# Optimization experiments

Measured on AMD Instinct MI355X. Metric: run time of the kernel, lower is better.

## Reference

```python
import jax, jax.numpy as jnp
import numpy as np

DIM = 768
B, N = 8, 2048
TEMPERATURE = 3.0


def setup_inputs() -> dict:
    key = jax.random.key(0)
    ks = jax.random.split(key, 5)
    lim = 1.0 / np.sqrt(DIM)
    x = jax.random.normal(ks[0], (B, N, DIM), dtype=jnp.float32)
    # torch Linear params: weight [out, in], bias [out]
    w_qkv = jax.random.uniform(ks[1], (3 * DIM, DIM), minval=-lim, maxval=lim, dtype=jnp.float32)
    b_qkv = jax.random.uniform(ks[2], (3 * DIM,), minval=-lim, maxval=lim, dtype=jnp.float32)
    w_proj = jax.random.uniform(ks[3], (DIM, DIM), minval=-lim, maxval=lim, dtype=jnp.float32)
    b_proj = jax.random.uniform(ks[4], (DIM,), minval=-lim, maxval=lim, dtype=jnp.float32)
    return {"x": x, "w_qkv": w_qkv, "b_qkv": b_qkv, "w_proj": w_proj, "b_proj": b_proj}


def reference(x, w_qkv, b_qkv, w_proj, b_proj):
    scale = DIM ** (-0.5)
    qkv = jnp.einsum('bnd,ed->bne', x, w_qkv) + b_qkv  # [b, n, 3*dim]
    q, k, v = jnp.split(qkv, 3, axis=-1)
    scores = jnp.einsum('bnd,bmd->bnm', q, k) * scale  # [b, n, n]
    attn = jax.nn.softmax(scores / TEMPERATURE, axis=-1)
    # dropout p=0.0 -> identity
    out = jnp.einsum('bnm,bmd->bnd', attn, v)
    return jnp.einsum('bnd,ed->bne', out, w_proj) + b_proj
```

## Files before the change

kernel.cpp:

```cpp
#include <hip/hip_runtime.h>
#include <hip/hip_bf16.h>
#include <math.h>

#define B_BATCH 8
#define SEQ 2048
#define DIM 768
#define E3 2304

typedef __bf16 bf16x8 __attribute__((ext_vector_type(8)));
typedef float floatx4 __attribute__((ext_vector_type(4)));

__device__ __forceinline__ void load_lds_16B(const __hip_bfloat16* g, __hip_bfloat16* l) {
    __builtin_amdgcn_global_load_lds((const __attribute__((address_space(1))) void*)g,
                                     (__attribute__((address_space(3))) void*)l, 16, 0, 0);
}

template<typename T> __device__ __forceinline__ T to_out(float v);
template<> __device__ __forceinline__ float to_out<float>(float v) { return v; }
template<> __device__ __forceinline__ __hip_bfloat16 to_out<__hip_bfloat16>(float v) { return __float2bfloat16(v); }

__global__ __launch_bounds__(256, 4)
void cvt_f32_bf16(const float* __restrict__ in, __hip_bfloat16* __restrict__ out, long n8)
{
    const long i = (long)blockIdx.x * blockDim.x + threadIdx.x;
    if (i >= n8) return;
    const float4* p = (const float4*)in + i * 2;
    const float4 a = p[0], b = p[1];
    union { uint4 u; __hip_bfloat16 h[8]; } t;
    t.h[0] = __float2bfloat16(a.x); t.h[1] = __float2bfloat16(a.y);
    t.h[2] = __float2bfloat16(a.z); t.h[3] = __float2bfloat16(a.w);
    t.h[4] = __float2bfloat16(b.x); t.h[5] = __float2bfloat16(b.y);
    t.h[6] = __float2bfloat16(b.z); t.h[7] = __float2bfloat16(b.w);
    ((uint4*)out)[i] = t.u;
}

__global__ __launch_bounds__(256, 4)
void transpose64(const __hip_bfloat16* __restrict__ in, long ldi, long si,
                 __hip_bfloat16* __restrict__ out, long ldo, long so)
{
    __shared__ __hip_bfloat16 t[64][65];
    in  += (long)blockIdx.z * si;
    out += (long)blockIdx.z * so;
    const int r0 = blockIdx.x * 64;
    const int c0 = blockIdx.y * 64;
    const int tid = threadIdx.x;
    const int r  = tid >> 3;
    const int c8 = (tid & 7) * 8;
#pragma unroll
    for (int h = 0; h < 2; ++h) {
        const int row = r + h * 32;
        union { uint4 u; __hip_bfloat16 v[8]; } tmp;
        tmp.u = *(const uint4*)(in + (long)(r0 + row) * ldi + c0 + c8);
#pragma unroll
        for (int j = 0; j < 8; ++j) t[row][c8 + j] = tmp.v[j];
    }
    __syncthreads();
#pragma unroll
    for (int h = 0; h < 2; ++h) {
        const int cr = r + h * 32;
        union { uint4 u; __hip_bfloat16 v[8]; } tmp;
#pragma unroll
        for (int j = 0; j < 8; ++j) tmp.v[j] = t[c8 + j][cr];
        *(uint4*)(out + (long)(c0 + cr) * ldo + r0 + c8) = tmp.u;
    }
}

template<typename OutT, int EPI>
__global__ __launch_bounds__(256, 2)
void gemm128(const __hip_bfloat16* __restrict__ A, long lda, long sA,
             const __hip_bfloat16* __restrict__ Bm, long ldb, long sB,
             OutT* __restrict__ C, long ldc, long sC,
             const float* __restrict__ bias, float scale, int K,
             int MB, int NB)
{
    __shared__ __hip_bfloat16 As[128 * 32];
    __shared__ __hip_bfloat16 Bs[128 * 32];
    __shared__ float lsum[128];

    const int id    = blockIdx.x;
    const int xcd   = id & 7;
    const int jj    = id >> 3;
    const int pairs = gridDim.x / NB;
    const int ppx   = pairs >> 3;
    const int pair  = xcd * ppx + jj / NB;
    const int nblk  = jj % NB;
    const int zblk  = pair / MB;
    const int mblk  = pair % MB;

    A  += (long)zblk * sA;
    Bm += (long)zblk * sB;
    C  += (long)zblk * sC;

    const int n0   = nblk * 128;
    const int m0   = mblk * 128;
    const int tid  = threadIdx.x;
    const int wave = tid >> 6;
    const int lane = tid & 63;
    const int wm   = (wave & 1) * 64;
    const int wn   = (wave >> 1) * 64;

    const int sr = lane >> 2;
    const int sc = (lane & 3) * 8;

    const int fr = lane & 15;
    const int fk = (lane >> 4) * 8;

    floatx4 acc[4][4] = {};
    float rsum[4] = {0.f, 0.f, 0.f, 0.f};

    for (int k0 = 0; k0 < K; k0 += 32) {
#pragma unroll
        for (int c = 0; c < 2; ++c) {
            const int chunk = wave * 2 + c;
            const int row   = chunk * 16 + sr;
            load_lds_16B(A  + (long)(m0 + row) * lda + (k0 + sc), As + chunk * 512);
            load_lds_16B(Bm + (long)(n0 + row) * ldb + (k0 + sc), Bs + chunk * 512);
        }
        __syncthreads();

        bf16x8 af[4], bfr[4];
#pragma unroll
        for (int i = 0; i < 4; ++i) {
            af[i]  = *(const bf16x8*)(As + (wm + i * 16 + fr) * 32 + fk);
            bfr[i] = *(const bf16x8*)(Bs + (wn + i * 16 + fr) * 32 + fk);
        }
        if constexpr (EPI == 2) {
#pragma unroll
            for (int mi = 0; mi < 4; ++mi)
#pragma unroll
                for (int j = 0; j < 8; ++j)
                    rsum[mi] += (float)af[mi][j];
        }
#pragma unroll
        for (int mi = 0; mi < 4; ++mi)
#pragma unroll
            for (int ni = 0; ni < 4; ++ni)
                acc[mi][ni] = __builtin_amdgcn_mfma_f32_16x16x32_bf16(
                    af[mi], bfr[ni], acc[mi][ni], 0, 0, 0);
        __syncthreads();
    }

    if constexpr (EPI == 2) {
#pragma unroll
        for (int mi = 0; mi < 4; ++mi) {
            rsum[mi] += __shfl_xor(rsum[mi], 16, 64);
            rsum[mi] += __shfl_xor(rsum[mi], 32, 64);
        }
        if (wave < 2 && (lane >> 4) == 0) {
#pragma unroll
            for (int mi = 0; mi < 4; ++mi)
                lsum[wm + mi * 16 + (lane & 15)] = rsum[mi];
        }
        __syncthreads();
    }

    const int cr = (lane >> 4) * 4;
    const int cc = lane & 15;

    float inv[4][4];
    if constexpr (EPI == 2) {
#pragma unroll
        for (int mi = 0; mi < 4; ++mi)
#pragma unroll
            for (int r = 0; r < 4; ++r)
                inv[mi][r] = 1.0f / lsum[wm + mi * 16 + cr + r];
    }

#pragma unroll
    for (int ni = 0; ni < 4; ++ni) {
        const int col = n0 + wn + ni * 16 + cc;
        const float bv = (EPI == 0 && bias) ? bias[col] : 0.0f;
#pragma unroll
        for (int mi = 0; mi < 4; ++mi) {
#pragma unroll
            for (int r = 0; r < 4; ++r) {
                const int row = m0 + wm + mi * 16 + cr + r;
                float v = acc[mi][ni][r];
                if constexpr (EPI == 0)      v = v * scale + bv;
                else if constexpr (EPI == 1) v = __expf(v * scale);
                else                         v = v * inv[mi][r];
                C[(long)row * ldc + col] = to_out<OutT>(v);
            }
        }
    }
}

extern "C" void kernel_launch(void* const* d_in, const int* in_sizes, int n_in,
                              void* d_out, int out_size, void* d_ws, size_t ws_size,
                              hipStream_t stream)
{
    const float* x     = (const float*)d_in[0];
    const float* w_qkv = (const float*)d_in[1];
    const float* b_qkv = (const float*)d_in[2];
    const float* w_prj = (const float*)d_in[3];
    const float* b_prj = (const float*)d_in[4];
    float* out = (float*)d_out;

    const float alpha = 1.0f / (sqrtf((float)DIM) * 3.0f);

    const size_t XE   = (size_t)B_BATCH * SEQ * DIM;
    const size_t WQE  = (size_t)E3 * DIM;
    const size_t WPE  = (size_t)DIM * DIM;
    const size_t QKVE = (size_t)B_BATCH * SEQ * E3;
    const size_t SE   = (size_t)B_BATCH * SEQ * SEQ;
    const size_t OE   = XE;
    dim3 blk(256);

    const size_t full_bytes = (XE + WQE + WPE + QKVE + SE + OE) * sizeof(__hip_bfloat16);

    if (ws_size >= full_bytes) {
        __hip_bfloat16* xb  = (__hip_bfloat16*)d_ws;
        __hip_bfloat16* wqb = xb + XE;
        __hip_bfloat16* wpb = wqb + WQE;
        __hip_bfloat16* qkv = wpb + WPE;
        __hip_bfloat16* S   = qkv + QKVE;
        __hip_bfloat16* O   = S + SE;
        __hip_bfloat16* Vt  = xb;

        cvt_f32_bf16<<<dim3((XE / 8 + 255) / 256), blk, 0, stream>>>(x, xb, XE / 8);
        cvt_f32_bf16<<<dim3((WQE / 8 + 255) / 256), blk, 0, stream>>>(w_qkv, wqb, WQE / 8);
        cvt_f32_bf16<<<dim3((WPE / 8 + 255) / 256), blk, 0, stream>>>(w_prj, wpb, WPE / 8);

        gemm128<__hip_bfloat16, 0><<<dim3(128 * 18), blk, 0, stream>>>(
            xb, DIM, 0, wqb, DIM, 0, qkv, E3, 0, b_qkv, 1.0f, DIM, 128, 18);
        transpose64<<<dim3(SEQ / 64, DIM / 64, B_BATCH), blk, 0, stream>>>(
            qkv + 2 * DIM, E3, (long)SEQ * E3, Vt, SEQ, (long)DIM * SEQ);
        gemm128<__hip_bfloat16, 1><<<dim3(16 * 16 * B_BATCH), blk, 0, stream>>>(
            qkv, E3, (long)SEQ * E3, qkv + DIM, E3, (long)SEQ * E3,
            S, SEQ, (long)SEQ * SEQ, nullptr, alpha, DIM, 16, 16);
        gemm128<__hip_bfloat16, 2><<<dim3(16 * 6 * B_BATCH), blk, 0, stream>>>(
            S, SEQ, (long)SEQ * SEQ, Vt, SEQ, (long)DIM * SEQ,
            O, DIM, (long)SEQ * DIM, nullptr, 1.0f, SEQ, 16, 6);
        gemm128<float, 0><<<dim3(128 * 6), blk, 0, stream>>>(
            O, DIM, 0, wpb, DIM, 0, out, DIM, 0, b_prj, 1.0f, DIM, 128, 6);
    } else {
        const size_t xE  = (size_t)SEQ * DIM;
        const size_t qE  = (size_t)SEQ * E3;
        const size_t sE1 = (size_t)SEQ * SEQ;
        __hip_bfloat16* wqb = (__hip_bfloat16*)d_ws;
        __hip_bfloat16* wpb = wqb + WQE;
        __hip_bfloat16* xb  = wpb + WPE;
        __hip_bfloat16* qkv = xb + xE;
        __hip_bfloat16* S   = qkv + qE;
        __hip_bfloat16* O   = S + sE1;
        __hip_bfloat16* Vt  = xb;

        cvt_f32_bf16<<<dim3((WQE / 8 + 255) / 256), blk, 0, stream>>>(w_qkv, wqb, WQE / 8);
        cvt_f32_bf16<<<dim3((WPE / 8 + 255) / 256), blk, 0, stream>>>(w_prj, wpb, WPE / 8);

        for (int b = 0; b < B_BATCH; ++b) {
            const float* xf = x + (size_t)b * xE;
            cvt_f32_bf16<<<dim3((xE / 8 + 255) / 256), blk, 0, stream>>>(xf, xb, xE / 8);
            gemm128<__hip_bfloat16, 0><<<dim3(16 * 18), blk, 0, stream>>>(
                xb, DIM, 0, wqb, DIM, 0, qkv, E3, 0, b_qkv, 1.0f, DIM, 16, 18);
            transpose64<<<dim3(SEQ / 64, DIM / 64, 1), blk, 0, stream>>>(
                qkv + 2 * DIM, E3, 0, Vt, SEQ, 0);
            gemm128<__hip_bfloat16, 1><<<dim3(16 * 16), blk, 0, stream>>>(
                qkv, E3, 0, qkv + DIM, E3, 0, S, SEQ, 0, nullptr, alpha, DIM, 16, 16);
            gemm128<__hip_bfloat16, 2><<<dim3(16 * 6), blk, 0, stream>>>(
                S, SEQ, 0, Vt, SEQ, 0, O, DIM, 0, nullptr, 1.0f, SEQ, 16, 6);
            gemm128<float, 0><<<dim3(16 * 6), blk, 0, stream>>>(
                O, DIM, 0, wpb, DIM, 0, out + (size_t)b * xE, DIM, 0, b_prj, 1.0f, DIM, 16, 6);
        }
    }
}
```

Baseline: 376.8 us.

## Replace 128-tile GEMM with 256x256 double-buffered, swizzled, 8-wave pipelined GEMM

Replaces the 128x128 tile GEMM (256 threads, single LDS buffer, K-step 32) with a 256x256 tile kernel using 512 threads, K-step 64 double-buffered LDS, XOR-swizzled LDS layout, and an interleaved schedule of global-to-LDS loads, fragment loads and MFMA quadrants with explicit barriers, vmcnt waits and setprio. The goal is more data reuse per tile, hiding global load latency behind MFMA work, and avoiding LDS bank conflicts. The larger tiles cut the grid size sharply (e.g. 192 workgroups for the output projection and the attention-times-V GEMM), which risks leaving many CUs idle. The 128 KB of LDS per block may also limit occupancy to one block per CU despite the launch bound of 2.

```diff
diff --git a/kernel.cpp b/kernel.cpp
--- a/kernel.cpp
+++ b/kernel.cpp
@@ -14,6 +14,10 @@
     __builtin_amdgcn_global_load_lds((const __attribute__((address_space(1))) void*)g,
                                      (__attribute__((address_space(3))) void*)l, 16, 0, 0);
 }
+
+#define MEMFENCE asm volatile("" ::: "memory")
+#define BAR() do { MEMFENCE; __builtin_amdgcn_s_barrier(); MEMFENCE; } while (0)
+#define WAITVM(N) asm volatile("s_waitcnt vmcnt(" #N ")" ::: "memory")
 
 template<typename T> __device__ __forceinline__ T to_out(float v);
 template<> __device__ __forceinline__ float to_out<float>(float v) { return v; }
@@ -65,122 +69,243 @@
     }
 }
 
+__device__ __forceinline__ void stage_half(const __hip_bfloat16* __restrict__ G, long ld,
+        int R0, int t, int h, __hip_bfloat16* lbuf, int wid, int lane)
+{
+    const int cs = ((lane & 7) ^ (lane >> 3)) << 3;
+#pragma unroll
+    for (int q = 0; q < 2; ++q) {
+        const int r = (q * 8 + wid) * 8 + (lane >> 3);
+        load_lds_16B(G + (long)(R0 + h * 128 + r) * ld + t * 64 + cs,
+                     lbuf + h * 8192 + (q * 8 + wid) * 512);
+    }
+}
+
+__device__ __forceinline__ bf16x8 ldfrag(const __hip_bfloat16* buf, int r, int kk, int g)
+{
+    const int o = r * 128 + ((kk * 64 + g * 16) ^ ((r & 7) << 4));
+    return *(const bf16x8*)((const char*)buf + o);
+}
+
+template<int QM>
+__device__ __forceinline__ void loadA(const __hip_bfloat16* SAb, bf16x8 (&af)[4][2],
+                                      int wrow, int fr, int g)
+{
+#pragma unroll
+    for (int mi = 0; mi < 4; ++mi)
+#pragma unroll
+        for (int kk = 0; kk < 2; ++kk)
+            af[mi][kk] = ldfrag(SAb, QM * 128 + wrow * 64 + mi * 16 + fr, kk, g);
+}
+
+template<int QN>
+__device__ __forceinline__ void loadB(const __hip_bfloat16* SBb, bf16x8 (&bf)[2][2],
+                                      int wcol, int fr, int g)
+{
+#pragma unroll
+    for (int ni = 0; ni < 2; ++ni)
+#pragma unroll
+        for (int kk = 0; kk < 2; ++kk)
+            bf[ni][kk] = ldfrag(SBb, QN * 128 + wcol * 32 + ni * 16 + fr, kk, g);
+}
+
+__device__ __forceinline__ void mfma16(const bf16x8 (&af)[4][2], const bf16x8 (&bf)[2][2],
+                                       floatx4 (&ac)[4][2])
+{
+#pragma unroll
+    for (int mi = 0; mi < 4; ++mi)
+#pragma unroll
+        for (int ni = 0; ni < 2; ++ni)
+#pragma unroll
+            for (int kk = 0; kk < 2; ++kk)
+                ac[mi][ni] = __builtin_amdgcn_mfma_f32_16x16x32_bf16(
+                    af[mi][kk], bf[ni][kk], ac[mi][ni], 0, 0, 0);
+}
+
+__device__ __forceinline__ void rsum_acc(const bf16x8 (&af)[4][2], float (&rs)[4])
+{
+#pragma unroll
+    for (int mi = 0; mi < 4; ++mi) {
+        float s = 0.f;
+#pragma unroll
+        for (int kk = 0; kk < 2; ++kk)
+#pragma unroll
+            for (int j = 0; j < 8; ++j)
+                s += (float)af[kk == 0 ? mi : mi][kk][j];
+        rs[mi] += s;
+    }
+}
+
 template<typename OutT, int EPI>
-__global__ __launch_bounds__(256, 2)
-void gemm128(const __hip_bfloat16* __restrict__ A, long lda, long sA,
+__global__ __launch_bounds__(512, 2)
+void gemm256(const __hip_bfloat16* __restrict__ A, long lda, long sA,
              const __hip_bfloat16* __restrict__ Bm, long ldb, long sB,
              OutT* __restrict__ C, long ldc, long sC,
              const float* __restrict__ bias, float scale, int K,
              int MB, int NB)
 {
-    __shared__ __hip_bfloat16 As[128 * 32];
-    __shared__ __hip_bfloat16 Bs[128 * 32];
-    __shared__ float lsum[128];
-
-    const int id    = blockIdx.x;
-    const int xcd   = id & 7;
-    const int jj    = id >> 3;
-    const int pairs = gridDim.x / NB;
-    const int ppx   = pairs >> 3;
-    const int pair  = xcd * ppx + jj / NB;
-    const int nblk  = jj % NB;
-    const int zblk  = pair / MB;
-    const int mblk  = pair % MB;
+    __shared__ __hip_bfloat16 SA[2][256 * 64];
+    __shared__ __hip_bfloat16 SB[2][256 * 64];
+    float* lsum = (float*)&SA[0][0];
+
+    const int nwg  = gridDim.x;
+    const int orig = blockIdx.x;
+    const int wgid = (orig & 7) * (nwg >> 3) + (orig >> 3);
+    const int zblk = wgid / (MB * NB);
+    const int rem  = wgid - zblk * (MB * NB);
+    const int mblk = rem / NB;
+    const int nblk = rem - mblk * NB;
 
     A  += (long)zblk * sA;
     Bm += (long)zblk * sB;
     C  += (long)zblk * sC;
-
-    const int n0   = nblk * 128;
-    const int m0   = mblk * 128;
+    const int m0 = mblk * 256, n0 = nblk * 256;
+
     const int tid  = threadIdx.x;
-    const int wave = tid >> 6;
-    const int lane = tid & 63;
-    const int wm   = (wave & 1) * 64;
-    const int wn   = (wave >> 1) * 64;
-
-    const int sr = lane >> 2;
-    const int sc = (lane & 3) * 8;
-
-    const int fr = lane & 15;
-    const int fk = (lane >> 4) * 8;
-
-    floatx4 acc[4][4] = {};
-    float rsum[4] = {0.f, 0.f, 0.f, 0.f};
-
-    for (int k0 = 0; k0 < K; k0 += 32) {
-#pragma unroll
-        for (int c = 0; c < 2; ++c) {
-            const int chunk = wave * 2 + c;
-            const int row   = chunk * 16 + sr;
-            load_lds_16B(A  + (long)(m0 + row) * lda + (k0 + sc), As + chunk * 512);
-            load_lds_16B(Bm + (long)(n0 + row) * ldb + (k0 + sc), Bs + chunk * 512);
+    const int wid  = tid >> 6, lane = tid & 63;
+    const int wrow = wid >> 2, wcol = wid & 3;
+    const int fr   = lane & 15, g = lane >> 4;
+
+    floatx4 acc[2][2][4][2] = {};
+    float   rsum[2][4] = {};
+    bf16x8  af[4][2], bfr[2][2][2];
+
+    const int NI = K >> 7;
+
+    stage_half(A,  lda, m0, 0, 0, SA[0], wid, lane);
+    stage_half(A,  lda, m0, 0, 1, SA[0], wid, lane);
+    stage_half(Bm, ldb, n0, 0, 0, SB[0], wid, lane);
+    stage_half(Bm, ldb, n0, 0, 1, SB[0], wid, lane);
+    stage_half(A,  lda, m0, 1, 0, SA[1], wid, lane);
+    stage_half(Bm, ldb, n0, 1, 0, SB[1], wid, lane);
+    WAITVM(4);
+    BAR();
+
+    for (int i = 0; i < NI; ++i) {
+        const int  t0   = 2 * i;
+        const bool last = (i == NI - 1);
+
+        loadA<0>(SA[0], af, wrow, fr, g);
+        loadB<0>(SB[0], bfr[0], wcol, fr, g);
+        stage_half(A,  lda, m0, t0 + 1, 1, SA[1], wid, lane);
+        stage_half(Bm, ldb, n0, t0 + 1, 1, SB[1], wid, lane);
+        BAR();
+        __builtin_amdgcn_s_setprio(1);
+        mfma16(af, bfr[0], acc[0][0]);
+        __builtin_amdgcn_s_setprio(0);
+        if constexpr (EPI == 2) rsum_acc(af, rsum[0]);
+        BAR();
+
+        loadB<1>(SB[0], bfr[1], wcol, fr, g);
+        BAR();
+        __builtin_amdgcn_s_setprio(1);
+        mfma16(af, bfr[1], acc[0][1]);
+        __builtin_amdgcn_s_setprio(0);
+        BAR();
+
+        loadA<1>(SA[0], af, wrow, fr, g);
+        if (!last) stage_half(A, lda, m0, t0 + 2, 0, SA[0], wid, lane);
+        BAR();
+        __builtin_amdgcn_s_setprio(1);
+        mfma16(af, bfr[0], acc[1][0]);
+        __builtin_amdgcn_s_setprio(0);
+        if constexpr (EPI == 2) rsum_acc(af, rsum[1]);
+        BAR();
+
+        if (!last) stage_half(Bm, ldb, n0, t0 + 2, 0, SB[0], wid, lane);
+        BAR();
+        __builtin_amdgcn_s_setprio(1);
+        mfma16(af, bfr[1], acc[1][1]);
+        __builtin_amdgcn_s_setprio(0);
+        if (!last) { WAITVM(4); } else { WAITVM(0); }
+        BAR();
+
+        loadA<0>(SA[1], af, wrow, fr, g);
+        loadB<0>(SB[1], bfr[0], wcol, fr, g);
+        if (!last) {
+            stage_half(A,  lda, m0, t0 + 2, 1, SA[0], wid, lane);
+            stage_half(Bm, ldb, n0, t0 + 2, 1, SB[0], wid, lane);
+        }
+        BAR();
+        __builtin_amdgcn_s_setprio(1);
+        mfma16(af, bfr[0], acc[0][0]);
+        __builtin_amdgcn_s_setprio(0);
+        if constexpr (EPI == 2) rsum_acc(af, rsum[0]);
+        BAR();
+
+        loadB<1>(SB[1], bfr[1], wcol, fr, g);
+        BAR();
+        __builtin_amdgcn_s_setprio(1);
+        mfma16(af, bfr[1], acc[0][1]);
+        __builtin_amdgcn_s_setprio(0);
+        BAR();
+
+        loadA<1>(SA[1], af, wrow, fr, g);
+        if (!last) stage_half(A, lda, m0, t0 + 3, 0, SA[1], wid, lane);
+        BAR();
+        __builtin_amdgcn_s_setprio(1);
+        mfma16(af, bfr[0], acc[1][0]);
+        __builtin_amdgcn_s_setprio(0);
+        if constexpr (EPI == 2) rsum_acc(af, rsum[1]);
+        BAR();
+
+        if (!last) stage_half(Bm, ldb, n0, t0 + 3, 0, SB[1], wid, lane);
+        BAR();
+        __builtin_amdgcn_s_setprio(1);
+        mfma16(af, bfr[1], acc[1][1]);
+        __builtin_amdgcn_s_setprio(0);
+        if (!last) WAITVM(4);
+        BAR();
+    }
+
+    if constexpr (EPI == 2) {
+#pragma unroll
+        for (int qm = 0; qm < 2; ++qm)
+#pragma unroll
+            for (int mi = 0; mi < 4; ++mi) {
+                rsum[qm][mi] += __shfl_xor(rsum[qm][mi], 16, 64);
+                rsum[qm][mi] += __shfl_xor(rsum[qm][mi], 32, 64);
+            }
+        if (wcol == 0 && g == 0) {
+#pragma unroll
+            for (int qm = 0; qm < 2; ++qm)
+#pragma unroll
+                for (int mi = 0; mi < 4; ++mi)
+                    lsum[qm * 128 + wrow * 64 + mi * 16 + fr] = rsum[qm][mi];
         }
         __syncthreads();
-
-        bf16x8 af[4], bfr[4];
-#pragma unroll
-        for (int i = 0; i < 4; ++i) {
-            af[i]  = *(const bf16x8*)(As + (wm + i * 16 + fr) * 32 + fk);
-            bfr[i] = *(const bf16x8*)(Bs + (wn + i * 16 + fr) * 32 + fk);
-        }
-        if constexpr (EPI == 2) {
+    }
+
+    const int cr = g * 4;
+    float inv[2][4][4];
+    if constexpr (EPI == 2) {
+#pragma unroll
+        for (int qm = 0; qm < 2; ++qm)
 #pragma unroll
             for (int mi = 0; mi < 4; ++mi)
 #pragma unroll
-                for (int j = 0; j < 8; ++j)
-                    rsum[mi] += (float)af[mi][j];
-        }
+                for (int r = 0; r < 4; ++r)
+                    inv[qm][mi][r] = 1.0f / lsum[qm * 128 + wrow * 64 + mi * 16 + cr + r];
+    }
+
+#pragma unroll
+    for (int qn = 0; qn < 2; ++qn)
+#pragma unroll
+    for (int ni = 0; ni < 2; ++ni) {
+        const int col = n0 + qn * 128 + wcol * 32 + ni * 16 + fr;
+        const float bv = (EPI == 0 && bias) ? bias[col] : 0.0f;
+#pragma unroll
+        for (int qm = 0; qm < 2; ++qm)
 #pragma unroll
         for (int mi = 0; mi < 4; ++mi)
 #pragma unroll
-            for (int ni = 0; ni < 4; ++ni)
-                acc[mi][ni] = __builtin_amdgcn_mfma_f32_16x16x32_bf16(
-                    af[mi], bfr[ni], acc[mi][ni], 0, 0, 0);
-        __syncthreads();
-    }
-
-    if constexpr (EPI == 2) {
-#pragma unroll
-        for (int mi = 0; mi < 4; ++mi) {
-            rsum[mi] += __shfl_xor(rsum[mi], 16, 64);
-            rsum[mi] += __shfl_xor(rsum[mi], 32, 64);
-        }
-        if (wave < 2 && (lane >> 4) == 0) {
-#pragma unroll
-            for (int mi = 0; mi < 4; ++mi)
-                lsum[wm + mi * 16 + (lane & 15)] = rsum[mi];
-        }
-        __syncthreads();
-    }
-
-    const int cr = (lane >> 4) * 4;
-    const int cc = lane & 15;
-
-    float inv[4][4];
-    if constexpr (EPI == 2) {
-#pragma unroll
-        for (int mi = 0; mi < 4; ++mi)
-#pragma unroll
-            for (int r = 0; r < 4; ++r)
-                inv[mi][r] = 1.0f / lsum[wm + mi * 16 + cr + r];
-    }
-
-#pragma unroll
-    for (int ni = 0; ni < 4; ++ni) {
-        const int col = n0 + wn + ni * 16 + cc;
-        const float bv = (EPI == 0 && bias) ? bias[col] : 0.0f;
-#pragma unroll
-        for (int mi = 0; mi < 4; ++mi) {
-#pragma unroll
-            for (int r = 0; r < 4; ++r) {
-                const int row = m0 + wm + mi * 16 + cr + r;
-                float v = acc[mi][ni][r];
-                if constexpr (EPI == 0)      v = v * scale + bv;
-                else if constexpr (EPI == 1) v = __expf(v * scale);
-                else                         v = v * inv[mi][r];
-                C[(long)row * ldc + col] = to_out<OutT>(v);
-            }
+        for (int r = 0; r < 4; ++r) {
+            const int row = m0 + qm * 128 + wrow * 64 + mi * 16 + cr + r;
+            float v = acc[qm][qn][mi][ni][r];
+            if constexpr (EPI == 0)      v = v * scale + bv;
+            else if constexpr (EPI == 1) v = __expf(v * scale);
+            else                         v = v * inv[qm][mi][r];
+            C[(long)row * ldc + col] = to_out<OutT>(v);
         }
     }
 }
@@ -204,7 +329,7 @@
     const size_t QKVE = (size_t)B_BATCH * SEQ * E3;
     const size_t SE   = (size_t)B_BATCH * SEQ * SEQ;
     const size_t OE   = XE;
-    dim3 blk(256);
+    dim3 blk(256), blkg(512);
 
     const size_t full_bytes = (XE + WQE + WPE + QKVE + SE + OE) * sizeof(__hip_bfloat16);
 
@@ -221,18 +346,18 @@
         cvt_f32_bf16<<<dim3((WQE / 8 + 255) / 256), blk, 0, stream>>>(w_qkv, wqb, WQE / 8);
         cvt_f32_bf16<<<dim3((WPE / 8 + 255) / 256), blk, 0, stream>>>(w_prj, wpb, WPE / 8);
 
-        gemm128<__hip_bfloat16, 0><<<dim3(128 * 18), blk, 0, stream>>>(
-            xb, DIM, 0, wqb, DIM, 0, qkv, E3, 0, b_qkv, 1.0f, DIM, 128, 18);
+        gemm256<__hip_bfloat16, 0><<<dim3(64 * 9), blkg, 0, stream>>>(
+            xb, DIM, 0, wqb, DIM, 0, qkv, E3, 0, b_qkv, 1.0f, DIM, 64, 9);
         transpose64<<<dim3(SEQ / 64, DIM / 64, B_BATCH), blk, 0, stream>>>(
             qkv + 2 * DIM, E3, (long)SEQ * E3, Vt, SEQ, (long)DIM * SEQ);
-        gemm128<__hip_bfloat16, 1><<<dim3(16 * 16 * B_BATCH), blk, 0, stream>>>(
+        gemm256<__hip_bfloat16, 1><<<dim3(8 * 8 * B_BATCH), blkg, 0, stream>>>(
             qkv, E3, (long)SEQ * E3, qkv + DIM, E3, (long)SEQ * E3,
-            S, SEQ, (long)SEQ * SEQ, nullptr, alpha, DIM, 16, 16);
-        gemm128<__hip_bfloat16, 2><<<dim3(16 * 6 * B_BATCH), blk, 0, stream>>>(
+            S, SEQ, (long)SEQ * SEQ, nullptr, alpha, DIM, 8, 8);
+        gemm256<__hip_bfloat16, 2><<<dim3(8 * 3 * B_BATCH), blkg, 0, stream>>>(
             S, SEQ, (long)SEQ * SEQ, Vt, SEQ, (long)DIM * SEQ,
-            O, DIM, (long)SEQ * DIM, nullptr, 1.0f, SEQ, 16, 6);
-        gemm128<float, 0><<<dim3(128 * 6), blk, 0, stream>>>(
-            O, DIM, 0, wpb, DIM, 0, out, DIM, 0, b_prj, 1.0f, DIM, 128, 6);
+            O, DIM, (long)SEQ * DIM, nullptr, 1.0f, SEQ, 8, 3);
+        gemm256<float, 0><<<dim3(64 * 3), blkg, 0, stream>>>(
+            O, DIM, 0, wpb, DIM, 0, out, DIM, 0, b_prj, 1.0f, DIM, 64, 3);
     } else {
         const size_t xE  = (size_t)SEQ * DIM;
         const size_t qE  = (size_t)SEQ * E3;
@@ -251,16 +376,16 @@
         for (int b = 0; b < B_BATCH; ++b) {
             const float* xf = x + (size_t)b * xE;
             cvt_f32_bf16<<<dim3((xE / 8 + 255) / 256), blk, 0, stream>>>(xf, xb, xE / 8);
-            gemm128<__hip_bfloat16, 0><<<dim3(16 * 18), blk, 0, stream>>>(
-                xb, DIM, 0, wqb, DIM, 0, qkv, E3, 0, b_qkv, 1.0f, DIM, 16, 18);
+            gemm256<__hip_bfloat16, 0><<<dim3(8 * 9), blkg, 0, stream>>>(
+                xb, DIM, 0, wqb, DIM, 0, qkv, E3, 0, b_qkv, 1.0f, DIM, 8, 9);
             transpose64<<<dim3(SEQ / 64, DIM / 64, 1), blk, 0, stream>>>(
                 qkv + 2 * DIM, E3, 0, Vt, SEQ, 0);
-            gemm128<__hip_bfloat16, 1><<<dim3(16 * 16), blk, 0, stream>>>(
-                qkv, E3, 0, qkv + DIM, E3, 0, S, SEQ, 0, nullptr, alpha, DIM, 16, 16);
-            gemm128<__hip_bfloat16, 2><<<dim3(16 * 6), blk, 0, stream>>>(
-                S, SEQ, 0, Vt, SEQ, 0, O, DIM, 0, nullptr, 1.0f, SEQ, 16, 6);
-            gemm128<float, 0><<<dim3(16 * 6), blk, 0, stream>>>(
-                O, DIM, 0, wpb, DIM, 0, out + (size_t)b * xE, DIM, 0, b_prj, 1.0f, DIM, 16, 6);
+            gemm256<__hip_bfloat16, 1><<<dim3(8 * 8), blkg, 0, stream>>>(
+                qkv, E3, 0, qkv + DIM, E3, 0, S, SEQ, 0, nullptr, alpha, DIM, 8, 8);
+            gemm256<__hip_bfloat16, 2><<<dim3(8 * 3), blkg, 0, stream>>>(
+                S, SEQ, 0, Vt, SEQ, 0, O, DIM, 0, nullptr, 1.0f, SEQ, 8, 3);
+            gemm256<float, 0><<<dim3(8 * 3), blkg, 0, stream>>>(
+                O, DIM, 0, wpb, DIM, 0, out + (size_t)b * xE, DIM, 0, b_prj, 1.0f, DIM, 8, 3);
         }
     }
 }
```

Measured after the change: 615.2 us. 1.63x slower.

## Replace 128x128 GEMM with 256x256 16-wave GEMM using 4-stage LDS pipeline

Applied to the files above, without the earlier changes.

Replaces the 256-thread 128x128 GEMM with a 1024-thread kernel computing 256x256 tiles. It uses a 4-deep ring of swizzled LDS buffers, explicit vmcnt waits and raw barriers to overlap global loads with MFMA work. The softmax row sums are now computed in the exp epilogue of the score GEMM via shuffles and global atomicAdd into a zeroed buffer, instead of summing bf16 A fragments inside the PV GEMM loop. This aims to raise data reuse and hide load latency. In exchange, grids become small (e.g. 192 workgroups for the PV and output GEMMs), occupancy drops to one workgroup per CU, and a memset plus atomics are added.

```diff
diff --git a/kernel.cpp b/kernel.cpp
--- a/kernel.cpp
+++ b/kernel.cpp
@@ -14,6 +14,10 @@
     __builtin_amdgcn_global_load_lds((const __attribute__((address_space(1))) void*)g,
                                      (__attribute__((address_space(3))) void*)l, 16, 0, 0);
 }
+
+#define MEMFENCE asm volatile("" ::: "memory")
+#define BAR() do { MEMFENCE; __builtin_amdgcn_s_barrier(); MEMFENCE; } while (0)
+#define WAITVM(N) asm volatile("s_waitcnt vmcnt(" #N ")" ::: "memory")
 
 template<typename T> __device__ __forceinline__ T to_out(float v);
 template<> __device__ __forceinline__ float to_out<float>(float v) { return v; }
@@ -65,97 +69,102 @@
     }
 }
 
+__device__ __forceinline__ floatx4 mfma_bf16(bf16x8 a, bf16x8 b, floatx4 c)
+{
+    return __builtin_amdgcn_mfma_f32_16x16x32_bf16(a, b, c, 0, 0, 0);
+}
+
 template<typename OutT, int EPI>
-__global__ __launch_bounds__(256, 2)
-void gemm128(const __hip_bfloat16* __restrict__ A, long lda, long sA,
+__global__ __launch_bounds__(1024, 1)
+void gemm16w(const __hip_bfloat16* __restrict__ A, long lda, long sA,
              const __hip_bfloat16* __restrict__ Bm, long ldb, long sB,
              OutT* __restrict__ C, long ldc, long sC,
-             const float* __restrict__ bias, float scale, int K,
-             int MB, int NB)
-{
-    __shared__ __hip_bfloat16 As[128 * 32];
-    __shared__ __hip_bfloat16 Bs[128 * 32];
-    __shared__ float lsum[128];
-
-    const int id    = blockIdx.x;
-    const int xcd   = id & 7;
-    const int jj    = id >> 3;
-    const int pairs = gridDim.x / NB;
-    const int ppx   = pairs >> 3;
-    const int pair  = xcd * ppx + jj / NB;
-    const int nblk  = jj % NB;
-    const int zblk  = pair / MB;
-    const int mblk  = pair % MB;
+             const float* __restrict__ bias,
+             float* __restrict__ rs, long srs,
+             float scale, int K, int MB, int NB)
+{
+    __shared__ __hip_bfloat16 SA[4][256 * 32];
+    __shared__ __hip_bfloat16 SB[4][256 * 32];
+
+    const int nwg  = gridDim.x;
+    const int orig = blockIdx.x;
+    const int wgid = (orig & 7) * (nwg >> 3) + (orig >> 3);
+    const int zblk = wgid / (MB * NB);
+    const int rem  = wgid - zblk * (MB * NB);
+    const int mblk = rem / NB;
+    const int nblk = rem - mblk * NB;
 
     A  += (long)zblk * sA;
     Bm += (long)zblk * sB;
     C  += (long)zblk * sC;
-
-    const int n0   = nblk * 128;
-    const int m0   = mblk * 128;
+    if constexpr (EPI != 0) rs += (long)zblk * srs;
+    const int m0 = mblk * 256, n0 = nblk * 256;
+
     const int tid  = threadIdx.x;
-    const int wave = tid >> 6;
-    const int lane = tid & 63;
-    const int wm   = (wave & 1) * 64;
-    const int wn   = (wave >> 1) * 64;
-
-    const int sr = lane >> 2;
-    const int sc = (lane & 3) * 8;
-
-    const int fr = lane & 15;
-    const int fk = (lane >> 4) * 8;
+    const int wid  = tid >> 6, lane = tid & 63;
+    const int wrow = wid >> 2, wcol = wid & 3;
+    const int fr   = lane & 15, g = lane >> 4;
+
+    const int grow = wid * 16 + (lane >> 2);
+    const int gcs  = (((lane & 3) - ((grow >> 1) & 3)) & 3) * 8;
+    const long offAst = (long)grow * lda + gcs;
+    const long offBst = (long)grow * ldb + gcs;
+    const __hip_bfloat16* Ag = A  + (long)m0 * lda;
+    const __hip_bfloat16* Bg = Bm + (long)n0 * ldb;
+
+    int offArd[4], offBrd[4];
+#pragma unroll
+    for (int i = 0; i < 4; ++i) {
+        const int ra = wrow * 64 + i * 16 + fr;
+        offArd[i] = ra * 64 + (((g + (ra >> 1)) & 3) << 4);
+        const int rb = wcol * 64 + i * 16 + fr;
+        offBrd[i] = rb * 64 + (((g + (rb >> 1)) & 3) << 4);
+    }
 
     floatx4 acc[4][4] = {};
-    float rsum[4] = {0.f, 0.f, 0.f, 0.f};
-
-    for (int k0 = 0; k0 < K; k0 += 32) {
-#pragma unroll
-        for (int c = 0; c < 2; ++c) {
-            const int chunk = wave * 2 + c;
-            const int row   = chunk * 16 + sr;
-            load_lds_16B(A  + (long)(m0 + row) * lda + (k0 + sc), As + chunk * 512);
-            load_lds_16B(Bm + (long)(n0 + row) * ldb + (k0 + sc), Bs + chunk * 512);
-        }
-        __syncthreads();
-
-        bf16x8 af[4], bfr[4];
-#pragma unroll
-        for (int i = 0; i < 4; ++i) {
-            af[i]  = *(const bf16x8*)(As + (wm + i * 16 + fr) * 32 + fk);
-            bfr[i] = *(const bf16x8*)(Bs + (wn + i * 16 + fr) * 32 + fk);
-        }
-        if constexpr (EPI == 2) {
+
+    const int NT = K >> 5;
+
+#define STG(t, buf) do { \
+        load_lds_16B(Ag + (long)(t) * 32 + offAst, &SA[buf][0] + wid * 512); \
+        load_lds_16B(Bg + (long)(t) * 32 + offBst, &SB[buf][0] + wid * 512); \
+    } while (0)
+
+    STG(0, 0); STG(1, 1); STG(2, 2);
+    WAITVM(4);
+    BAR();
+
+    for (int tb = 0; tb < NT; tb += 4) {
+#pragma unroll
+        for (int u = 0; u < 4; ++u) {
+            const int t = tb + u;
+            const char* sa = (const char*)&SA[u][0];
+            const char* sb = (const char*)&SB[u][0];
+            bf16x8 af[4], bf[4];
+#pragma unroll
+            for (int i = 0; i < 4; ++i) {
+                af[i] = *(const bf16x8*)(sa + offArd[i]);
+                bf[i] = *(const bf16x8*)(sb + offBrd[i]);
+            }
+            if (t + 3 < NT) STG(t + 3, (u + 3) & 3);
+            BAR();
+            __builtin_amdgcn_s_setprio(1);
 #pragma unroll
             for (int mi = 0; mi < 4; ++mi)
 #pragma unroll
-                for (int j = 0; j < 8; ++j)
-                    rsum[mi] += (float)af[mi][j];
-        }
-#pragma unroll
-        for (int mi = 0; mi < 4; ++mi)
-#pragma unroll
-            for (int ni = 0; ni < 4; ++ni)
-                acc[mi][ni] = __builtin_amdgcn_mfma_f32_16x16x32_bf16(
-                    af[mi], bfr[ni], acc[mi][ni], 0, 0, 0);
-        __syncthreads();
-    }
-
-    if constexpr (EPI == 2) {
-#pragma unroll
-        for (int mi = 0; mi < 4; ++mi) {
-            rsum[mi] += __shfl_xor(rsum[mi], 16, 64);
-            rsum[mi] += __shfl_xor(rsum[mi], 32, 64);
-        }
-        if (wave < 2 && (lane >> 4) == 0) {
-#pragma unroll
-            for (int mi = 0; mi < 4; ++mi)
-                lsum[wm + mi * 16 + (lane & 15)] = rsum[mi];
-        }
-        __syncthreads();
-    }
-
-    const int cr = (lane >> 4) * 4;
-    const int cc = lane & 15;
+                for (int ni = 0; ni < 4; ++ni)
+                    acc[mi][ni] = mfma_bf16(af[mi], bf[ni], acc[mi][ni]);
+            __builtin_amdgcn_s_setprio(0);
+            if (t < NT - 3)       { WAITVM(4); }
+            else if (t == NT - 3) { WAITVM(2); }
+            else if (t == NT - 2) { WAITVM(0); }
+            BAR();
+        }
+    }
+#undef STG
+
+    const int r0w = m0 + wrow * 64;
+    const int c0w = n0 + wcol * 64;
 
     float inv[4][4];
     if constexpr (EPI == 2) {
@@ -163,24 +172,40 @@
         for (int mi = 0; mi < 4; ++mi)
 #pragma unroll
             for (int r = 0; r < 4; ++r)
-                inv[mi][r] = 1.0f / lsum[wm + mi * 16 + cr + r];
-    }
+                inv[mi][r] = 1.0f / rs[r0w + mi * 16 + g * 4 + r];
+    }
+
+    float rsume[4][4] = {};
 
 #pragma unroll
     for (int ni = 0; ni < 4; ++ni) {
-        const int col = n0 + wn + ni * 16 + cc;
+        const int col = c0w + ni * 16 + fr;
         const float bv = (EPI == 0 && bias) ? bias[col] : 0.0f;
 #pragma unroll
-        for (int mi = 0; mi < 4; ++mi) {
-#pragma unroll
-            for (int r = 0; r < 4; ++r) {
-                const int row = m0 + wm + mi * 16 + cr + r;
-                float v = acc[mi][ni][r];
-                if constexpr (EPI == 0)      v = v * scale + bv;
-                else if constexpr (EPI == 1) v = __expf(v * scale);
-                else                         v = v * inv[mi][r];
-                C[(long)row * ldc + col] = to_out<OutT>(v);
-            }
+        for (int mi = 0; mi < 4; ++mi)
+#pragma unroll
+        for (int r = 0; r < 4; ++r) {
+            const int row = r0w + mi * 16 + g * 4 + r;
+            float v = acc[mi][ni][r];
+            if constexpr (EPI == 0)      v = v * scale + bv;
+            else if constexpr (EPI == 1) { v = __expf(v * scale); rsume[mi][r] += v; }
+            else                         v = v * inv[mi][r];
+            C[(long)row * ldc + col] = to_out<OutT>(v);
+        }
+    }
+
+    if constexpr (EPI == 1) {
+#pragma unroll
+        for (int mi = 0; mi < 4; ++mi)
+#pragma unroll
+        for (int r = 0; r < 4; ++r) {
+            float s = rsume[mi][r];
+            s += __shfl_xor(s, 1, 64);
+            s += __shfl_xor(s, 2, 64);
+            s += __shfl_xor(s, 4, 64);
+            s += __shfl_xor(s, 8, 64);
+            if (fr == 0)
+                atomicAdd(&rs[r0w + mi * 16 + g * 4 + r], s);
         }
     }
 }
@@ -204,9 +229,11 @@
     const size_t QKVE = (size_t)B_BATCH * SEQ * E3;
     const size_t SE   = (size_t)B_BATCH * SEQ * SEQ;
     const size_t OE   = XE;
-    dim3 blk(256);
-
-    const size_t full_bytes = (XE + WQE + WPE + QKVE + SE + OE) * sizeof(__hip_bfloat16);
+    const size_t RSE  = (size_t)B_BATCH * SEQ;
+    dim3 blk(256), blkg(1024);
+
+    const size_t full_bytes = (XE + WQE + WPE + QKVE + SE + OE) * sizeof(__hip_bfloat16)
+                            + RSE * sizeof(float);
 
     if (ws_size >= full_bytes) {
         __hip_bfloat16* xb  = (__hip_bfloat16*)d_ws;
@@ -215,24 +242,26 @@
         __hip_bfloat16* qkv = wpb + WPE;
         __hip_bfloat16* S   = qkv + QKVE;
         __hip_bfloat16* O   = S + SE;
+        float*          RS  = (float*)(O + OE);
         __hip_bfloat16* Vt  = xb;
 
         cvt_f32_bf16<<<dim3((XE / 8 + 255) / 256), blk, 0, stream>>>(x, xb, XE / 8);
         cvt_f32_bf16<<<dim3((WQE / 8 + 255) / 256), blk, 0, stream>>>(w_qkv, wqb, WQE / 8);
         cvt_f32_bf16<<<dim3((WPE / 8 + 255) / 256), blk, 0, stream>>>(w_prj, wpb, WPE / 8);
-
-        gemm128<__hip_bfloat16, 0><<<dim3(128 * 18), blk, 0, stream>>>(
-            xb, DIM, 0, wqb, DIM, 0, qkv, E3, 0, b_qkv, 1.0f, DIM, 128, 18);
+        hipMemsetAsync(RS, 0, RSE * sizeof(float), stream);
+
+        gemm16w<__hip_bfloat16, 0><<<dim3(64 * 9), blkg, 0, stream>>>(
+            xb, DIM, 0, wqb, DIM, 0, qkv, E3, 0, b_qkv, nullptr, 0, 1.0f, DIM, 64, 9);
         transpose64<<<dim3(SEQ / 64, DIM / 64, B_BATCH), blk, 0, stream>>>(
             qkv + 2 * DIM, E3, (long)SEQ * E3, Vt, SEQ, (long)DIM * SEQ);
-        gemm128<__hip_bfloat16, 1><<<dim3(16 * 16 * B_BATCH), blk, 0, stream>>>(
+        gemm16w<__hip_bfloat16, 1><<<dim3(8 * 8 * B_BATCH), blkg, 0, stream>>>(
             qkv, E3, (long)SEQ * E3, qkv + DIM, E3, (long)SEQ * E3,
-            S, SEQ, (long)SEQ * SEQ, nullptr, alpha, DIM, 16, 16);
-        gemm128<__hip_bfloat16, 2><<<dim3(16 * 6 * B_BATCH), blk, 0, stream>>>(
+            S, SEQ, (long)SEQ * SEQ, nullptr, RS, SEQ, alpha, DIM, 8, 8);
+        gemm16w<__hip_bfloat16, 2><<<dim3(8 * 3 * B_BATCH), blkg, 0, stream>>>(
             S, SEQ, (long)SEQ * SEQ, Vt, SEQ, (long)DIM * SEQ,
-            O, DIM, (long)SEQ * DIM, nullptr, 1.0f, SEQ, 16, 6);
-        gemm128<float, 0><<<dim3(128 * 6), blk, 0, stream>>>(
-            O, DIM, 0, wpb, DIM, 0, out, DIM, 0, b_prj, 1.0f, DIM, 128, 6);
+            O, DIM, (long)SEQ * DIM, nullptr, RS, SEQ, 1.0f, SEQ, 8, 3);
+        gemm16w<float, 0><<<dim3(64 * 3), blkg, 0, stream>>>(
+            O, DIM, 0, wpb, DIM, 0, out, DIM, 0, b_prj, nullptr, 0, 1.0f, DIM, 64, 3);
     } else {
         const size_t xE  = (size_t)SEQ * DIM;
         const size_t qE  = (size_t)SEQ * E3;
@@ -243,6 +272,7 @@
         __hip_bfloat16* qkv = xb + xE;
         __hip_bfloat16* S   = qkv + qE;
         __hip_bfloat16* O   = S + sE1;
+        float*          RS  = (float*)(O + xE);
         __hip_bfloat16* Vt  = xb;
 
         cvt_f32_bf16<<<dim3((WQE / 8 + 255) / 256), blk, 0, stream>>>(w_qkv, wqb, WQE / 8);
@@ -251,16 +281,17 @@
         for (int b = 0; b < B_BATCH; ++b) {
             const float* xf = x + (size_t)b * xE;
             cvt_f32_bf16<<<dim3((xE / 8 + 255) / 256), blk, 0, stream>>>(xf, xb, xE / 8);
-            gemm128<__hip_bfloat16, 0><<<dim3(16 * 18), blk, 0, stream>>>(
-                xb, DIM, 0, wqb, DIM, 0, qkv, E3, 0, b_qkv, 1.0f, DIM, 16, 18);
+            hipMemsetAsync(RS, 0, SEQ * sizeof(float), stream);
+            gemm16w<__hip_bfloat16, 0><<<dim3(8 * 9), blkg, 0, stream>>>(
+                xb, DIM, 0, wqb, DIM, 0, qkv, E3, 0, b_qkv, nullptr, 0, 1.0f, DIM, 8, 9);
             transpose64<<<dim3(SEQ / 64, DIM / 64, 1), blk, 0, stream>>>(
                 qkv + 2 * DIM, E3, 0, Vt, SEQ, 0);
-            gemm128<__hip_bfloat16, 1><<<dim3(16 * 16), blk, 0, stream>>>(
-                qkv, E3, 0, qkv + DIM, E3, 0, S, SEQ, 0, nullptr, alpha, DIM, 16, 16);
-            gemm128<__hip_bfloat16, 2><<<dim3(16 * 6), blk, 0, stream>>>(
-                S, SEQ, 0, Vt, SEQ, 0, O, DIM, 0, nullptr, 1.0f, SEQ, 16, 6);
-            gemm128<float, 0><<<dim3(16 * 6), blk, 0, stream>>>(
-                O, DIM, 0, wpb, DIM, 0, out + (size_t)b * xE, DIM, 0, b_prj, 1.0f, DIM, 16, 6);
-        }
-    }
-}
+            gemm16w<__hip_bfloat16, 1><<<dim3(8 * 8), blkg, 0, stream>>>(
+                qkv, E3, 0, qkv + DIM, E3, 0, S, SEQ, 0, nullptr, RS, 0, alpha, DIM, 8, 8);
+            gemm16w<__hip_bfloat16, 2><<<dim3(8 * 3), blkg, 0, stream>>>(
+                S, SEQ, 0, Vt, SEQ, 0, O, DIM, 0, nullptr, RS, 0, 1.0f, SEQ, 8, 3);
+            gemm16w<float, 0><<<dim3(8 * 3), blkg, 0, stream>>>(
+                O, DIM, 0, wpb, DIM, 0, out + (size_t)b * xE, DIM, 0, b_prj, nullptr, 0, 1.0f, DIM, 8, 3);
+        }
+    }
+}
```

After: 395.9 us. +5.1%, slower.

## Compute softmax row sums in exp GEMM epilogue via atomics and swizzle LDS

Applied to the files above, without the earlier changes.

Moves the softmax row-sum computation out of the attention-times-V GEMM inner loop. The exp epilogue of the score GEMM now reduces each row's partial sums across lanes and atomically adds them into a global float buffer, which is zeroed with a memset beforehand. It also XOR-style rotates the k-chunk placement in LDS to cut bank conflicts on fragment reads, and reorders the epilogue loops so row-wise values are hoisted. The cost is extra atomics and a memset, and the row sums now come from fp32 exp values rather than the rounded bf16 values, which changes numerics slightly.

```diff
diff --git a/kernel.cpp b/kernel.cpp
--- a/kernel.cpp
+++ b/kernel.cpp
@@ -70,12 +70,12 @@
 void gemm128(const __hip_bfloat16* __restrict__ A, long lda, long sA,
              const __hip_bfloat16* __restrict__ Bm, long ldb, long sB,
              OutT* __restrict__ C, long ldc, long sC,
-             const float* __restrict__ bias, float scale, int K,
-             int MB, int NB)
+             const float* __restrict__ bias,
+             float* __restrict__ rs, long srs,
+             float scale, int K, int MB, int NB)
 {
     __shared__ __hip_bfloat16 As[128 * 32];
     __shared__ __hip_bfloat16 Bs[128 * 32];
-    __shared__ float lsum[128];
 
     const int id    = blockIdx.x;
     const int xcd   = id & 7;
@@ -90,6 +90,7 @@
     A  += (long)zblk * sA;
     Bm += (long)zblk * sB;
     C  += (long)zblk * sC;
+    if constexpr (EPI != 0) rs += (long)zblk * srs;
 
     const int n0   = nblk * 128;
     const int m0   = mblk * 128;
@@ -99,37 +100,30 @@
     const int wm   = (wave & 1) * 64;
     const int wn   = (wave >> 1) * 64;
 
-    const int sr = lane >> 2;
-    const int sc = (lane & 3) * 8;
-
-    const int fr = lane & 15;
-    const int fk = (lane >> 4) * 8;
+    const int sr  = lane >> 2;
+    const int scs = ((((lane & 3) - ((sr >> 1) & 3)) & 3)) * 8;
+
+    const int fr  = lane & 15;
+    const int g   = lane >> 4;
+    const int fks = ((g + (fr >> 1)) & 3) * 8;
 
     floatx4 acc[4][4] = {};
-    float rsum[4] = {0.f, 0.f, 0.f, 0.f};
 
     for (int k0 = 0; k0 < K; k0 += 32) {
 #pragma unroll
         for (int c = 0; c < 2; ++c) {
             const int chunk = wave * 2 + c;
             const int row   = chunk * 16 + sr;
-            load_lds_16B(A  + (long)(m0 + row) * lda + (k0 + sc), As + chunk * 512);
-            load_lds_16B(Bm + (long)(n0 + row) * ldb + (k0 + sc), Bs + chunk * 512);
+            load_lds_16B(A  + (long)(m0 + row) * lda + (k0 + scs), As + chunk * 512);
+            load_lds_16B(Bm + (long)(n0 + row) * ldb + (k0 + scs), Bs + chunk * 512);
         }
         __syncthreads();
 
         bf16x8 af[4], bfr[4];
 #pragma unroll
         for (int i = 0; i < 4; ++i) {
-            af[i]  = *(const bf16x8*)(As + (wm + i * 16 + fr) * 32 + fk);
-            bfr[i] = *(const bf16x8*)(Bs + (wn + i * 16 + fr) * 32 + fk);
-        }
-        if constexpr (EPI == 2) {
-#pragma unroll
-            for (int mi = 0; mi < 4; ++mi)
-#pragma unroll
-                for (int j = 0; j < 8; ++j)
-                    rsum[mi] += (float)af[mi][j];
+            af[i]  = *(const bf16x8*)(As + (wm + i * 16 + fr) * 32 + fks);
+            bfr[i] = *(const bf16x8*)(Bs + (wn + i * 16 + fr) * 32 + fks);
         }
 #pragma unroll
         for (int mi = 0; mi < 4; ++mi)
@@ -140,46 +134,38 @@
         __syncthreads();
     }
 
-    if constexpr (EPI == 2) {
-#pragma unroll
-        for (int mi = 0; mi < 4; ++mi) {
-            rsum[mi] += __shfl_xor(rsum[mi], 16, 64);
-            rsum[mi] += __shfl_xor(rsum[mi], 32, 64);
-        }
-        if (wave < 2 && (lane >> 4) == 0) {
-#pragma unroll
-            for (int mi = 0; mi < 4; ++mi)
-                lsum[wm + mi * 16 + (lane & 15)] = rsum[mi];
-        }
-        __syncthreads();
-    }
-
-    const int cr = (lane >> 4) * 4;
-    const int cc = lane & 15;
-
-    float inv[4][4];
-    if constexpr (EPI == 2) {
-#pragma unroll
-        for (int mi = 0; mi < 4; ++mi)
-#pragma unroll
-            for (int r = 0; r < 4; ++r)
-                inv[mi][r] = 1.0f / lsum[wm + mi * 16 + cr + r];
-    }
-
-#pragma unroll
-    for (int ni = 0; ni < 4; ++ni) {
-        const int col = n0 + wn + ni * 16 + cc;
-        const float bv = (EPI == 0 && bias) ? bias[col] : 0.0f;
-#pragma unroll
-        for (int mi = 0; mi < 4; ++mi) {
-#pragma unroll
-            for (int r = 0; r < 4; ++r) {
-                const int row = m0 + wm + mi * 16 + cr + r;
+    const int cr = g * 4;
+
+    float bv[4];
+    if constexpr (EPI == 0) {
+#pragma unroll
+        for (int ni = 0; ni < 4; ++ni)
+            bv[ni] = bias ? bias[n0 + wn + ni * 16 + fr] : 0.0f;
+    }
+
+#pragma unroll
+    for (int mi = 0; mi < 4; ++mi) {
+#pragma unroll
+        for (int r = 0; r < 4; ++r) {
+            const int row = m0 + wm + mi * 16 + cr + r;
+            float invv;
+            if constexpr (EPI == 2) invv = 1.0f / rs[row];
+            float s = 0.0f;
+#pragma unroll
+            for (int ni = 0; ni < 4; ++ni) {
+                const int col = n0 + wn + ni * 16 + fr;
                 float v = acc[mi][ni][r];
-                if constexpr (EPI == 0)      v = v * scale + bv;
-                else if constexpr (EPI == 1) v = __expf(v * scale);
-                else                         v = v * inv[mi][r];
+                if constexpr (EPI == 0)      v = v * scale + bv[ni];
+                else if constexpr (EPI == 1) { v = __expf(v * scale); s += v; }
+                else                         v = v * invv;
                 C[(long)row * ldc + col] = to_out<OutT>(v);
+            }
+            if constexpr (EPI == 1) {
+                s += __shfl_xor(s, 1, 64);
+                s += __shfl_xor(s, 2, 64);
+                s += __shfl_xor(s, 4, 64);
+                s += __shfl_xor(s, 8, 64);
+                if (fr == 0) atomicAdd(&rs[row], s);
             }
         }
     }
@@ -204,9 +190,11 @@
     const size_t QKVE = (size_t)B_BATCH * SEQ * E3;
     const size_t SE   = (size_t)B_BATCH * SEQ * SEQ;
     const size_t OE   = XE;
+    const size_t RSE  = (size_t)B_BATCH * SEQ;
     dim3 blk(256);
 
-    const size_t full_bytes = (XE + WQE + WPE + QKVE + SE + OE) * sizeof(__hip_bfloat16);
+    const size_t full_bytes = (XE + WQE + WPE + QKVE + SE + OE) * sizeof(__hip_bfloat16)
+                            + RSE * sizeof(float);
 
     if (ws_size >= full_bytes) {
         __hip_bfloat16* xb  = (__hip_bfloat16*)d_ws;
@@ -215,24 +203,26 @@
         __hip_bfloat16* qkv = wpb + WPE;
         __hip_bfloat16* S   = qkv + QKVE;
         __hip_bfloat16* O   = S + SE;
+        float*          RS  = (float*)(O + OE);
         __hip_bfloat16* Vt  = xb;
 
         cvt_f32_bf16<<<dim3((XE / 8 + 255) / 256), blk, 0, stream>>>(x, xb, XE / 8);
         cvt_f32_bf16<<<dim3((WQE / 8 + 255) / 256), blk, 0, stream>>>(w_qkv, wqb, WQE / 8);
         cvt_f32_bf16<<<dim3((WPE / 8 + 255) / 256), blk, 0, stream>>>(w_prj, wpb, WPE / 8);
+        hipMemsetAsync(RS, 0, RSE * sizeof(float), stream);
 
         gemm128<__hip_bfloat16, 0><<<dim3(128 * 18), blk, 0, stream>>>(
-            xb, DIM, 0, wqb, DIM, 0, qkv, E3, 0, b_qkv, 1.0f, DIM, 128, 18);
+            xb, DIM, 0, wqb, DIM, 0, qkv, E3, 0, b_qkv, nullptr, 0, 1.0f, DIM, 128, 18);
         transpose64<<<dim3(SEQ / 64, DIM / 64, B_BATCH), blk, 0, stream>>>(
             qkv + 2 * DIM, E3, (long)SEQ * E3, Vt, SEQ, (long)DIM * SEQ);
         gemm128<__hip_bfloat16, 1><<<dim3(16 * 16 * B_BATCH), blk, 0, stream>>>(
             qkv, E3, (long)SEQ * E3, qkv + DIM, E3, (long)SEQ * E3,
-            S, SEQ, (long)SEQ * SEQ, nullptr, alpha, DIM, 16, 16);
+            S, SEQ, (long)SEQ * SEQ, nullptr, RS, SEQ, alpha, DIM, 16, 16);
         gemm128<__hip_bfloat16, 2><<<dim3(16 * 6 * B_BATCH), blk, 0, stream>>>(
             S, SEQ, (long)SEQ * SEQ, Vt, SEQ, (long)DIM * SEQ,
-            O, DIM, (long)SEQ * DIM, nullptr, 1.0f, SEQ, 16, 6);
+            O, DIM, (long)SEQ * DIM, nullptr, RS, SEQ, 1.0f, SEQ, 16, 6);
         gemm128<float, 0><<<dim3(128 * 6), blk, 0, stream>>>(
-            O, DIM, 0, wpb, DIM, 0, out, DIM, 0, b_prj, 1.0f, DIM, 128, 6);
+            O, DIM, 0, wpb, DIM, 0, out, DIM, 0, b_prj, nullptr, 0, 1.0f, DIM, 128, 6);
     } else {
         const size_t xE  = (size_t)SEQ * DIM;
         const size_t qE  = (size_t)SEQ * E3;
@@ -243,6 +233,7 @@
         __hip_bfloat16* qkv = xb + xE;
         __hip_bfloat16* S   = qkv + qE;
         __hip_bfloat16* O   = S + sE1;
+        float*          RS  = (float*)(O + xE);
         __hip_bfloat16* Vt  = xb;
 
         cvt_f32_bf16<<<dim3((WQE / 8 + 255) / 256), blk, 0, stream>>>(w_qkv, wqb, WQE / 8);
@@ -251,16 +242,17 @@
         for (int b = 0; b < B_BATCH; ++b) {
             const float* xf = x + (size_t)b * xE;
             cvt_f32_bf16<<<dim3((xE / 8 + 255) / 256), blk, 0, stream>>>(xf, xb, xE / 8);
+            hipMemsetAsync(RS, 0, SEQ * sizeof(float), stream);
             gemm128<__hip_bfloat16, 0><<<dim3(16 * 18), blk, 0, stream>>>(
-                xb, DIM, 0, wqb, DIM, 0, qkv, E3, 0, b_qkv, 1.0f, DIM, 16, 18);
+                xb, DIM, 0, wqb, DIM, 0, qkv, E3, 0, b_qkv, nullptr, 0, 1.0f, DIM, 16, 18);
             transpose64<<<dim3(SEQ / 64, DIM / 64, 1), blk, 0, stream>>>(
                 qkv + 2 * DIM, E3, 0, Vt, SEQ, 0);
             gemm128<__hip_bfloat16, 1><<<dim3(16 * 16), blk, 0, stream>>>(
-                qkv, E3, 0, qkv + DIM, E3, 0, S, SEQ, 0, nullptr, alpha, DIM, 16, 16);
+                qkv, E3, 0, qkv + DIM, E3, 0, S, SEQ, 0, nullptr, RS, 0, alpha, DIM, 16, 16);
             gemm128<__hip_bfloat16, 2><<<dim3(16 * 6), blk, 0, stream>>>(
-                S, SEQ, 0, Vt, SEQ, 0, O, DIM, 0, nullptr, 1.0f, SEQ, 16, 6);
+                S, SEQ, 0, Vt, SEQ, 0, O, DIM, 0, nullptr, RS, 0, 1.0f, SEQ, 16, 6);
             gemm128<float, 0><<<dim3(16 * 6), blk, 0, stream>>>(
-                O, DIM, 0, wpb, DIM, 0, out + (size_t)b * xE, DIM, 0, b_prj, 1.0f, DIM, 16, 6);
-        }
-    }
-}
+                O, DIM, 0, wpb, DIM, 0, out + (size_t)b * xE, DIM, 0, b_prj, nullptr, 0, 1.0f, DIM, 16, 6);
+        }
+    }
+}
```

New measurement: 368.3 us. -2.2%, faster.
